# Kernel optimization log

Hardware: AMD Instinct MI355X
Metric: run time of the kernel (lower is better)

The kernel has to match this reference:

```python
import jax, jax.numpy as jnp
import numpy as np
import math

B, T, C = 4, 2048, 1024
H = 16
DH = C // H
SCALE = 1.0 / math.sqrt(DH)


def setup_inputs() -> dict:
    key = jax.random.key(0)
    k1, k2, k3 = jax.random.split(key, 3)
    x = jax.random.normal(k1, (B, T, C), dtype=jnp.float32)
    # init_unit_norm: randn / sqrt(d_in)
    W_qkv = jax.random.normal(k2, (3 * C, C), dtype=jnp.float32) / math.sqrt(C)
    W_out = jax.random.normal(k3, (C, C), dtype=jnp.float32) / math.sqrt(C)
    return {"x": x, "W_qkv": W_qkv, "W_out": W_out}


def reference(x, W_qkv, W_out):
    b, t, c = x.shape
    qkv = x @ W_qkv.T                      # [B,T,3C]
    q, k, v = jnp.split(qkv, 3, axis=-1)
    # [B,T,C] -> [B,H,T,Dh]
    q = q.reshape(b, t, H, DH).transpose(0, 2, 1, 3)
    k = k.reshape(b, t, H, DH).transpose(0, 2, 1, 3)
    v = v.reshape(b, t, H, DH).transpose(0, 2, 1, 3)
    scores = jnp.einsum('bhtd,bhsd->bhts', q, k) * SCALE  # [B,H,T,T]
    mask = jnp.tril(jnp.ones((t, t), dtype=bool))
    scores = jnp.where(mask, scores, 0.0)  # no softmax
    attn = jnp.einsum('bhts,bhsd->bhtd', scores, v)       # [B,H,T,Dh]
    attn = attn.transpose(0, 2, 1, 3).reshape(b, t, c)
    return attn @ W_out.T
```

## Files before the change

kernel.cpp:

```cpp
#include <hip/hip_runtime.h>

#define TT 2048
#define CC 1024

typedef __attribute__((ext_vector_type(8))) __bf16 bf16x8;
typedef __attribute__((ext_vector_type(4))) float f32x4;
typedef unsigned int u32;

__device__ __forceinline__ short f2bf(float f) {
  u32 u = __float_as_uint(f);
  u += 0x7fffu + ((u >> 16) & 1u);
  return (short)(u >> 16);
}

#if __has_builtin(__builtin_amdgcn_cvt_pk_bf16_f32)
__device__ __forceinline__ u32 pack2(float a, float b) {
  auto v = __builtin_amdgcn_cvt_pk_bf16_f32(a, b);
  return __builtin_bit_cast(u32, v);
}
#else
__device__ __forceinline__ u32 pack2(float a, float b) {
  u32 ua = __float_as_uint(a), ub = __float_as_uint(b);
  ua += 0x7fffu + ((ua >> 16) & 1u);
  ub += 0x7fffu + ((ub >> 16) & 1u);
  return (ua >> 16) | (ub & 0xffff0000u);
}
#endif

__global__ __launch_bounds__(256) void cvt_all(const float* __restrict__ x,
                                               const float* __restrict__ wqkv,
                                               const float* __restrict__ wout,
                                               short* __restrict__ dst) {
  int i = blockIdx.x * blockDim.x + threadIdx.x;
  const float* src;
  float sc = 1.0f;
  if (i < 2097152) {
    src = x + (size_t)i * 4;
  } else if (i < 2883584) {
    int j = i - 2097152;
    src = wqkv + (size_t)j * 4;
    if (j < 262144) sc = 0.125f;
  } else {
    src = wout + (size_t)(i - 2883584) * 4;
  }
  float4 f = *reinterpret_cast<const float4*>(src);
  short4 s;
  s.x = f2bf(f.x * sc); s.y = f2bf(f.y * sc); s.z = f2bf(f.z * sc); s.w = f2bf(f.w * sc);
  reinterpret_cast<short4*>(dst)[i] = s;
}

__device__ __forceinline__ void storev(float* p, float v) { *p = v; }
__device__ __forceinline__ void storev(short* p, float v) { *p = f2bf(v); }

#if __has_builtin(__builtin_amdgcn_global_load_lds)
#define HAVE_GLD_LDS 1
__device__ __forceinline__ void gld_lds16(const short* g, short* l) {
  __builtin_amdgcn_global_load_lds((const __attribute__((address_space(1))) u32*)g,
                                   (__attribute__((address_space(3))) u32*)l, 16, 0, 0);
}
#endif

template <typename OutT>
__global__ __launch_bounds__(256) void gemm_bt(const short* __restrict__ A,
                                               const short* __restrict__ B,
                                               OutT* __restrict__ Cm,
                                               int M, int N, int K) {
  __shared__ __align__(16) short As[128 * 32];
  __shared__ __align__(16) short Bs[128 * 32];
  const int tid = threadIdx.x;
  const int wave = tid >> 6, lane = tid & 63;
  const int quad = lane >> 4, nl = lane & 15;
  const int m0 = blockIdx.x * 128, n0 = blockIdx.y * 128;
  const int wr = (wave >> 1) * 64, wc = (wave & 1) * 64;
  f32x4 acc[4][4] = {};
  for (int k0 = 0; k0 < K; k0 += 32) {
    __syncthreads();
#pragma unroll
    for (int i = 0; i < 2; ++i) {
      int idx = tid + i * 256;
      int row = idx >> 2, cg = idx & 3;
#if HAVE_GLD_LDS
      gld_lds16(&A[(size_t)(m0 + row) * K + k0 + cg * 8], &As[(i * 256 + wave * 64) * 8]);
      gld_lds16(&B[(size_t)(n0 + row) * K + k0 + cg * 8], &Bs[(i * 256 + wave * 64) * 8]);
#else
      *reinterpret_cast<uint4*>(&As[row * 32 + cg * 8]) =
          *reinterpret_cast<const uint4*>(&A[(size_t)(m0 + row) * K + k0 + cg * 8]);
      *reinterpret_cast<uint4*>(&Bs[row * 32 + cg * 8]) =
          *reinterpret_cast<const uint4*>(&B[(size_t)(n0 + row) * K + k0 + cg * 8]);
#endif
    }
    __syncthreads();
    bf16x8 af[4], bfr[4];
#pragma unroll
    for (int i = 0; i < 4; ++i)
      af[i] = *reinterpret_cast<const bf16x8*>(&As[(wr + i * 16 + nl) * 32 + quad * 8]);
#pragma unroll
    for (int i = 0; i < 4; ++i)
      bfr[i] = *reinterpret_cast<const bf16x8*>(&Bs[(wc + i * 16 + nl) * 32 + quad * 8]);
#pragma unroll
    for (int mi = 0; mi < 4; ++mi)
#pragma unroll
      for (int ni = 0; ni < 4; ++ni)
        acc[mi][ni] = __builtin_amdgcn_mfma_f32_16x16x32_bf16(af[mi], bfr[ni], acc[mi][ni], 0, 0, 0);
  }
#pragma unroll
  for (int mi = 0; mi < 4; ++mi)
#pragma unroll
    for (int ni = 0; ni < 4; ++ni) {
      int row = m0 + wr + mi * 16 + quad * 4;
      int col = n0 + wc + ni * 16 + nl;
#pragma unroll
      for (int r = 0; r < 4; ++r)
        storev(&Cm[(size_t)(row + r) * N + col], acc[mi][ni][r]);
    }
}

__global__ __launch_bounds__(256) void transpose_v(const short* __restrict__ qkv,
                                                   short* __restrict__ vt) {
  __shared__ short Ls[64 * 68];
  const int bh = blockIdx.y, tb = blockIdx.x;
  const int b = bh >> 4, h = bh & 15;
  const int tid = threadIdx.x;
  const short* src = qkv + (size_t)(b * TT + tb * 64) * (3 * CC) + 2 * CC + h * 64;
#pragma unroll
  for (int i = 0; i < 2; ++i) {
    int idx = tid + i * 256;
    int tl = idx >> 3, dc = idx & 7;
    uint4 d4 = *reinterpret_cast<const uint4*>(&src[(size_t)tl * (3 * CC) + dc * 8]);
    *reinterpret_cast<uint2*>(&Ls[tl * 68 + dc * 8]) = make_uint2(d4.x, d4.y);
    *reinterpret_cast<uint2*>(&Ls[tl * 68 + dc * 8 + 4]) = make_uint2(d4.z, d4.w);
  }
  __syncthreads();
  short* dst = vt + (size_t)(bh * 64) * TT + tb * 64;
#pragma unroll
  for (int i = 0; i < 2; ++i) {
    int idx = tid + i * 256;
    int dl = idx >> 3, tc = idx & 7;
    short tmp[8];
#pragma unroll
    for (int j = 0; j < 8; ++j) tmp[j] = Ls[(tc * 8 + j) * 68 + dl];
    *reinterpret_cast<uint4*>(&dst[(size_t)dl * TT + tc * 8]) = *reinterpret_cast<uint4*>(tmp);
  }
}

__device__ __forceinline__ f32x4 mfma16(bf16x8 a, bf16x8 b, f32x4 c) {
  return __builtin_amdgcn_mfma_f32_16x16x32_bf16(a, b, c, 0, 0, 0);
}

template <bool DIAG>
__device__ __forceinline__ void attn_compute(const short* kf, const short* vf, u32* ssw,
                                             const bf16x8 (&qf)[2][2], f32x4 (&o)[2][4],
                                             int lane, int quad, int nl) {
  bf16x8 k00 = *reinterpret_cast<const bf16x8*>(&kf[0 * 512 + lane * 8]);
  bf16x8 k01 = *reinterpret_cast<const bf16x8*>(&kf[1 * 512 + lane * 8]);
  bf16x8 k10 = *reinterpret_cast<const bf16x8*>(&kf[2 * 512 + lane * 8]);
  bf16x8 k11 = *reinterpret_cast<const bf16x8*>(&kf[3 * 512 + lane * 8]);
  bf16x8 vB[4];
#pragma unroll
  for (int nb = 0; nb < 4; ++nb)
    vB[nb] = *reinterpret_cast<const bf16x8*>(&vf[nb * 512 + lane * 8]);
  {
    u32* srow = &ssw[0 * 320 + nl * 20];
    f32x4 s0 = {};
    s0 = mfma16(k00, qf[0][0], s0);
    s0 = mfma16(k01, qf[0][1], s0);
    if (DIAG) {
#pragma unroll
      for (int r = 0; r < 4; ++r) s0[r] = (quad * 4 + r <= nl) ? s0[r] : 0.0f;
    }
#pragma unroll
    for (int p = 0; p < 2; ++p) srow[quad * 2 + p] = pack2(s0[2 * p], s0[2 * p + 1]);
    if (DIAG) {
#pragma unroll
      for (int p = 0; p < 2; ++p) srow[8 + quad * 2 + p] = 0;
    } else {
      f32x4 s1 = {};
      s1 = mfma16(k10, qf[0][0], s1);
      s1 = mfma16(k11, qf[0][1], s1);
#pragma unroll
      for (int p = 0; p < 2; ++p) srow[8 + quad * 2 + p] = pack2(s1[2 * p], s1[2 * p + 1]);
    }
  }
  {
    u32* srow = &ssw[1 * 320 + nl * 20];
    f32x4 s0 = {}, s1 = {};
    s0 = mfma16(k00, qf[1][0], s0);
    s0 = mfma16(k01, qf[1][1], s0);
    s1 = mfma16(k10, qf[1][0], s1);
    s1 = mfma16(k11, qf[1][1], s1);
    if (DIAG) {
#pragma unroll
      for (int r = 0; r < 4; ++r) s1[r] = (quad * 4 + r <= nl) ? s1[r] : 0.0f;
    }
#pragma unroll
    for (int p = 0; p < 2; ++p) {
      srow[quad * 2 + p] = pack2(s0[2 * p], s0[2 * p + 1]);
      srow[8 + quad * 2 + p] = pack2(s1[2 * p], s1[2 * p + 1]);
    }
  }
#pragma unroll
  for (int m = 0; m < 2; ++m) {
    bf16x8 sf = *reinterpret_cast<const bf16x8*>(&ssw[m * 320 + nl * 20 + quad * 4]);
#pragma unroll
    for (int nb = 0; nb < 4; ++nb) o[m][nb] = mfma16(sf, vB[nb], o[m][nb]);
  }
}

__global__ __launch_bounds__(256, 3) void attn_kernel(const short* __restrict__ qkv,
                                                      const short* __restrict__ vt,
                                                      short* __restrict__ attnb) {
  const int bh = blockIdx.x;
  const int b = bh >> 4, h = bh & 15;
  const int ti = 15 - blockIdx.y;
  const int T0 = ti * 128;
  const int tid = threadIdx.x;
  const int wave = tid >> 6, lane = tid & 63;
  const int quad = lane >> 4, nl = lane & 15;

  const short* qbase = qkv + (size_t)(b * TT) * (3 * CC) + h * 64;
  const short* kbase = qbase + CC;
  const short* vbase = vt + (size_t)(bh * 64) * TT;

  __shared__ __align__(16) short Frag[2][8192];
  __shared__ __align__(16) u32 Ss[4][640];
  u32* ssw = Ss[wave];

  const int tw0 = T0 + wave * 32;
  bf16x8 qf[2][2];
#pragma unroll
  for (int m = 0; m < 2; ++m)
#pragma unroll
    for (int half = 0; half < 2; ++half)
      qf[m][half] = *reinterpret_cast<const bf16x8*>(
          &qbase[(size_t)(tw0 + m * 16 + nl) * (3 * CC) + half * 32 + quad * 8]);

  f32x4 o[2][4] = {};

  const short* ksrc = kbase + (size_t)(wave * 16 + nl) * (3 * CC) + quad * 8;
  const int sp_w = wave >> 1, nb0 = (wave & 1) * 2;
  const short* vsrc0 = vbase + (size_t)((nb0 + 0) * 16 + nl) * TT + sp_w * 32 + quad * 8;
  const short* vsrc1 = vbase + (size_t)((nb0 + 1) * 16 + nl) * TT + sp_w * 32 + quad * 8;

  auto stage = [&](short* fb, int c) {
    const size_t koff = (size_t)(c * 64) * (3 * CC);
#if HAVE_GLD_LDS
    gld_lds16(ksrc + koff, &fb[(2 * wave) * 512]);
    gld_lds16(ksrc + koff + 32, &fb[(2 * wave + 1) * 512]);
    gld_lds16(vsrc0 + c * 64, &fb[4096 + (2 * wave) * 512]);
    gld_lds16(vsrc1 + c * 64, &fb[4096 + (2 * wave + 1) * 512]);
#else
    *reinterpret_cast<uint4*>(&fb[(2 * wave) * 512 + lane * 8]) =
        *reinterpret_cast<const uint4*>(ksrc + koff);
    *reinterpret_cast<uint4*>(&fb[(2 * wave + 1) * 512 + lane * 8]) =
        *reinterpret_cast<const uint4*>(ksrc + koff + 32);
    *reinterpret_cast<uint4*>(&fb[4096 + (2 * wave) * 512 + lane * 8]) =
        *reinterpret_cast<const uint4*>(vsrc0 + c * 64);
    *reinterpret_cast<uint4*>(&fb[4096 + (2 * wave + 1) * 512 + lane * 8]) =
        *reinterpret_cast<const uint4*>(vsrc1 + c * 64);
#endif
  };

  const int nch = 2 * ti + 2;
  const int cd = 4 * ti + wave;

  stage(Frag[0], 0);
  for (int c = 0; c < nch; ++c) {
    __syncthreads();
    if (c + 1 < nch) stage(Frag[(c + 1) & 1], c + 1);
    const short* fb = Frag[c & 1];
    const int c0 = 2 * c, c1 = 2 * c + 1;
    if (c0 < cd)
      attn_compute<false>(fb, fb + 4096, ssw, qf, o, lane, quad, nl);
    else if (c0 == cd)
      attn_compute<true>(fb, fb + 4096, ssw, qf, o, lane, quad, nl);
    if (c1 < cd)
      attn_compute<false>(fb + 2048, fb + 4096 + 2048, ssw, qf, o, lane, quad, nl);
    else if (c1 == cd)
      attn_compute<true>(fb + 2048, fb + 4096 + 2048, ssw, qf, o, lane, quad, nl);
  }

#pragma unroll
  for (int m = 0; m < 2; ++m)
#pragma unroll
    for (int nb = 0; nb < 4; ++nb)
#pragma unroll
      for (int r = 0; r < 4; ++r) {
        int t = tw0 + m * 16 + quad * 4 + r;
        attnb[(size_t)(b * TT + t) * CC + h * 64 + nb * 16 + nl] = f2bf(o[m][nb][r]);
      }
}

extern "C" void kernel_launch(void* const* d_in, const int* in_sizes, int n_in,
                              void* d_out, int out_size, void* d_ws, size_t ws_size,
                              hipStream_t stream) {
  const float* x = (const float*)d_in[0];
  const float* wqkv = (const float*)d_in[1];
  const float* wout = (const float*)d_in[2];
  float* out = (float*)d_out;

  char* ws = (char*)d_ws;
  short* xb    = (short*)(ws);
  short* wqkvb = (short*)(ws + 16777216);
  short* woutb = (short*)(ws + 23068672);
  short* qkvb  = (short*)(ws + 25165824);
  short* attnb = (short*)(ws + 75497472);
  short* vt    = xb;

  cvt_all<<<12288, 256, 0, stream>>>(x, wqkv, wout, xb);

  gemm_bt<short><<<dim3(64, 24), 256, 0, stream>>>(xb, wqkvb, qkvb, 8192, 3072, 1024);

  transpose_v<<<dim3(32, 64), 256, 0, stream>>>(qkvb, vt);

  attn_kernel<<<dim3(64, 16), 256, 0, stream>>>(qkvb, vt, attnb);

  gemm_bt<float><<<dim3(64, 8), 256, 0, stream>>>(attnb, woutb, out, 8192, 1024, 1024);
}
```

Measured before the change: 251.4 us.

## Replace GEMM with 256x256 tiled, double-buffered, ping-pong scheduled MFMA kernel

Replaces the 128x128 single-buffered GEMM with a 512-thread, 256x256-tile kernel. It uses 128KB of dynamic LDS with double buffering, XOR-swizzled LDS layout, grouped workgroup remapping for L2 reuse, and phased barriers with setprio so MFMA work overlaps the direct global-to-LDS loads. The aim is to cut the load stalls and barrier overhead of the old synchronous k-loop and to raise data reuse per tile. In exchange, the large LDS footprint limits occupancy, and the larger tiles give fewer workgroups (128 for the output projection), which may underfill the GPU.

```diff
diff --git a/kernel.cpp b/kernel.cpp
--- a/kernel.cpp
+++ b/kernel.cpp
@@ -60,59 +60,145 @@
 }
 #endif
 
-template <typename OutT>
-__global__ __launch_bounds__(256) void gemm_bt(const short* __restrict__ A,
-                                               const short* __restrict__ B,
-                                               OutT* __restrict__ Cm,
-                                               int M, int N, int K) {
-  __shared__ __align__(16) short As[128 * 32];
-  __shared__ __align__(16) short Bs[128 * 32];
+__device__ __forceinline__ f32x4 mfma16(bf16x8 a, bf16x8 b, f32x4 c) {
+  return __builtin_amdgcn_mfma_f32_16x16x32_bf16(a, b, c, 0, 0, 0);
+}
+
+template <int MH>
+__device__ __forceinline__ void mma4x4(f32x4 (&acc)[8][4], const bf16x8 (&af)[4],
+                                       const bf16x8 (&bfr)[4]) {
+#pragma unroll
+  for (int mf = 0; mf < 4; ++mf)
+#pragma unroll
+    for (int nf = 0; nf < 4; ++nf)
+      acc[MH * 4 + mf][nf] = mfma16(af[mf], bfr[nf], acc[MH * 4 + mf][nf]);
+}
+
+#define GPHASE(DB, KS, MH, LOADB, STG, SYNC)               \
+  {                                                        \
+    ldA(af, DB, KS, MH);                                   \
+    if (LOADB) ldB(bfr, DB, KS);                           \
+    STG;                                                   \
+    __builtin_amdgcn_s_barrier();                          \
+    asm volatile("s_waitcnt lgkmcnt(0)" ::: "memory");     \
+    __builtin_amdgcn_sched_barrier(0);                     \
+    __builtin_amdgcn_s_setprio(1);                         \
+    mma4x4<MH>(acc, af, bfr);                              \
+    __builtin_amdgcn_s_setprio(0);                         \
+    SYNC;                                                  \
+    __builtin_amdgcn_s_barrier();                          \
+  }
+#define SYNC6 asm volatile("s_waitcnt vmcnt(6)" ::: "memory")
+#define SYNC0 asm volatile("s_waitcnt vmcnt(0)" ::: "memory")
+#define GNOOP ((void)0)
+
+template <typename OutT, int N, int K>
+__global__ __launch_bounds__(512, 2) void gemm256(const short* __restrict__ A,
+                                                  const short* __restrict__ B,
+                                                  OutT* __restrict__ Cm) {
+  extern __shared__ short lds[];
+  constexpr int NT = K / 64;
+  constexpr int NITER = NT / 2;
+  constexpr int NWG = (N / 256) * 32;
   const int tid = threadIdx.x;
   const int wave = tid >> 6, lane = tid & 63;
   const int quad = lane >> 4, nl = lane & 15;
-  const int m0 = blockIdx.x * 128, n0 = blockIdx.y * 128;
-  const int wr = (wave >> 1) * 64, wc = (wave & 1) * 64;
-  f32x4 acc[4][4] = {};
-  for (int k0 = 0; k0 < K; k0 += 32) {
-    __syncthreads();
-#pragma unroll
-    for (int i = 0; i < 2; ++i) {
-      int idx = tid + i * 256;
-      int row = idx >> 2, cg = idx & 3;
+  const int wm = wave >> 2, wn = wave & 3;
+
+  int id = blockIdx.y * 32 + blockIdx.x;
+  id = (id & 7) * (NWG / 8) + (id >> 3);
+  const int m0 = (id & 31) * 256, n0 = (id >> 5) * 256;
+
+  const int srow = lane >> 2;
+  const int sperm = ((lane & 3) ^ ((lane >> 3) & 3)) * 8;
+  const short* pA = A + (size_t)(m0 + wave * 32 + srow) * K + sperm;
+  const short* pB = B + (size_t)(n0 + wave * 32 + srow) * K + sperm;
+  short* dstA = lds + wave * 1024;
+  short* dstB = lds + 16384 + wave * 1024;
+
+  const int perm = (quad ^ ((nl >> 1) & 3)) * 8;
+  const int aoff = (wm * 128 + nl) * 32 + perm;
+  const int boff = (wn * 64 + nl) * 32 + perm;
+
+  f32x4 acc[8][4] = {};
+
+  auto stageA = [&](int db, int ks, int t) {
+    const short* s = pA + (size_t)t * 64 + ks * 32;
+    short* d = dstA + db * 32768 + ks * 8192;
 #if HAVE_GLD_LDS
-      gld_lds16(&A[(size_t)(m0 + row) * K + k0 + cg * 8], &As[(i * 256 + wave * 64) * 8]);
-      gld_lds16(&B[(size_t)(n0 + row) * K + k0 + cg * 8], &Bs[(i * 256 + wave * 64) * 8]);
+    gld_lds16(s, d);
+    gld_lds16(s + (size_t)16 * K, d + 512);
 #else
-      *reinterpret_cast<uint4*>(&As[row * 32 + cg * 8]) =
-          *reinterpret_cast<const uint4*>(&A[(size_t)(m0 + row) * K + k0 + cg * 8]);
-      *reinterpret_cast<uint4*>(&Bs[row * 32 + cg * 8]) =
-          *reinterpret_cast<const uint4*>(&B[(size_t)(n0 + row) * K + k0 + cg * 8]);
+    *reinterpret_cast<uint4*>(d + lane * 8) = *reinterpret_cast<const uint4*>(s);
+    *reinterpret_cast<uint4*>(d + 512 + lane * 8) =
+        *reinterpret_cast<const uint4*>(s + (size_t)16 * K);
 #endif
+  };
+  auto stageB = [&](int db, int ks, int t) {
+    const short* s = pB + (size_t)t * 64 + ks * 32;
+    short* d = dstB + db * 32768 + ks * 8192;
+#if HAVE_GLD_LDS
+    gld_lds16(s, d);
+    gld_lds16(s + (size_t)16 * K, d + 512);
+#else
+    *reinterpret_cast<uint4*>(d + lane * 8) = *reinterpret_cast<const uint4*>(s);
+    *reinterpret_cast<uint4*>(d + 512 + lane * 8) =
+        *reinterpret_cast<const uint4*>(s + (size_t)16 * K);
+#endif
+  };
+  auto ldA = [&](bf16x8 (&af)[4], int db, int ks, int mh) {
+#pragma unroll
+    for (int mf = 0; mf < 4; ++mf)
+      af[mf] = *reinterpret_cast<const bf16x8*>(
+          &lds[db * 32768 + ks * 8192 + aoff + (mh * 4 + mf) * 512]);
+  };
+  auto ldB = [&](bf16x8 (&bfr)[4], int db, int ks) {
+#pragma unroll
+    for (int nf = 0; nf < 4; ++nf)
+      bfr[nf] = *reinterpret_cast<const bf16x8*>(
+          &lds[db * 32768 + 16384 + ks * 8192 + boff + nf * 512]);
+  };
+
+  stageA(0, 0, 0); stageA(0, 1, 0); stageB(0, 0, 0); stageB(0, 1, 0);
+  stageB(1, 0, 1); stageA(1, 0, 1); stageB(1, 1, 1);
+  asm volatile("s_waitcnt vmcnt(6)" ::: "memory");
+  __builtin_amdgcn_s_barrier();
+
+  for (int i = 0; i < NITER - 1; ++i) {
+    const int to1 = 2 * i + 1, te2 = 2 * i + 2, to3 = 2 * i + 3;
+    bf16x8 af[4], bfr[4];
+    GPHASE(0, 0, 0, 1, stageA(1, 1, to1), GNOOP)
+    GPHASE(0, 0, 1, 0, stageB(0, 0, te2), GNOOP)
+    GPHASE(0, 1, 0, 1, stageA(0, 0, te2), GNOOP)
+    GPHASE(0, 1, 1, 0, stageB(0, 1, te2), SYNC6)
+    GPHASE(1, 0, 0, 1, stageA(0, 1, te2), GNOOP)
+    GPHASE(1, 0, 1, 0, stageB(1, 0, to3), GNOOP)
+    GPHASE(1, 1, 0, 1, stageA(1, 0, to3), GNOOP)
+    GPHASE(1, 1, 1, 0, stageB(1, 1, to3), SYNC6)
+  }
+  {
+    bf16x8 af[4], bfr[4];
+    GPHASE(0, 0, 0, 1, stageA(1, 1, NT - 1), GNOOP)
+    GPHASE(0, 0, 1, 0, GNOOP, GNOOP)
+    GPHASE(0, 1, 0, 1, GNOOP, GNOOP)
+    GPHASE(0, 1, 1, 0, GNOOP, SYNC0)
+    GPHASE(1, 0, 0, 1, GNOOP, GNOOP)
+    GPHASE(1, 0, 1, 0, GNOOP, GNOOP)
+    GPHASE(1, 1, 0, 1, GNOOP, GNOOP)
+    GPHASE(1, 1, 1, 0, GNOOP, GNOOP)
+  }
+
+#pragma unroll
+  for (int mf = 0; mf < 8; ++mf) {
+    const int row = m0 + wm * 128 + mf * 16 + quad * 4;
+#pragma unroll
+    for (int nf = 0; nf < 4; ++nf) {
+      const int col = n0 + wn * 64 + nf * 16 + nl;
+#pragma unroll
+      for (int r = 0; r < 4; ++r)
+        storev(&Cm[(size_t)(row + r) * N + col], acc[mf][nf][r]);
     }
-    __syncthreads();
-    bf16x8 af[4], bfr[4];
-#pragma unroll
-    for (int i = 0; i < 4; ++i)
-      af[i] = *reinterpret_cast<const bf16x8*>(&As[(wr + i * 16 + nl) * 32 + quad * 8]);
-#pragma unroll
-    for (int i = 0; i < 4; ++i)
-      bfr[i] = *reinterpret_cast<const bf16x8*>(&Bs[(wc + i * 16 + nl) * 32 + quad * 8]);
-#pragma unroll
-    for (int mi = 0; mi < 4; ++mi)
-#pragma unroll
-      for (int ni = 0; ni < 4; ++ni)
-        acc[mi][ni] = __builtin_amdgcn_mfma_f32_16x16x32_bf16(af[mi], bfr[ni], acc[mi][ni], 0, 0, 0);
-  }
-#pragma unroll
-  for (int mi = 0; mi < 4; ++mi)
-#pragma unroll
-    for (int ni = 0; ni < 4; ++ni) {
-      int row = m0 + wr + mi * 16 + quad * 4;
-      int col = n0 + wc + ni * 16 + nl;
-#pragma unroll
-      for (int r = 0; r < 4; ++r)
-        storev(&Cm[(size_t)(row + r) * N + col], acc[mi][ni][r]);
-    }
+  }
 }
 
 __global__ __launch_bounds__(256) void transpose_v(const short* __restrict__ qkv,
@@ -141,10 +227,6 @@
     for (int j = 0; j < 8; ++j) tmp[j] = Ls[(tc * 8 + j) * 68 + dl];
     *reinterpret_cast<uint4*>(&dst[(size_t)dl * TT + tc * 8]) = *reinterpret_cast<uint4*>(tmp);
   }
-}
-
-__device__ __forceinline__ f32x4 mfma16(bf16x8 a, bf16x8 b, f32x4 c) {
-  return __builtin_amdgcn_mfma_f32_16x16x32_bf16(a, b, c, 0, 0, 0);
 }
 
 template <bool DIAG>
@@ -306,13 +388,22 @@
   short* attnb = (short*)(ws + 75497472);
   short* vt    = xb;
 
+  static bool inited = false;
+  if (!inited) {
+    hipFuncSetAttribute(reinterpret_cast<const void*>(&gemm256<short, 3072, 1024>),
+                        hipFuncAttributeMaxDynamicSharedMemorySize, 131072);
+    hipFuncSetAttribute(reinterpret_cast<const void*>(&gemm256<float, 1024, 1024>),
+                        hipFuncAttributeMaxDynamicSharedMemorySize, 131072);
+    inited = true;
+  }
+
   cvt_all<<<12288, 256, 0, stream>>>(x, wqkv, wout, xb);
 
-  gemm_bt<short><<<dim3(64, 24), 256, 0, stream>>>(xb, wqkvb, qkvb, 8192, 3072, 1024);
+  gemm256<short, 3072, 1024><<<dim3(32, 12), 512, 131072, stream>>>(xb, wqkvb, qkvb);
 
   transpose_v<<<dim3(32, 64), 256, 0, stream>>>(qkvb, vt);
 
   attn_kernel<<<dim3(64, 16), 256, 0, stream>>>(qkvb, vt, attnb);
 
-  gemm_bt<float><<<dim3(64, 8), 256, 0, stream>>>(attnb, woutb, out, 8192, 1024, 1024);
-}
+  gemm256<float, 1024, 1024><<<dim3(32, 4), 512, 131072, stream>>>(attnb, woutb, out);
+}
```

After: 243.1 us. 1.03x faster.
